# Kernel tuning notes

Measured on AMD Instinct MI355X. Metric: run time of the kernel, lower is better.

The kernel has to match this reference:

```python
import jax, jax.numpy as jnp
import numpy as np

FP, ENC, H, OUT, STEPS = 4860, 512, 512, 42, 128


def _lin(k, fan_in, fan_out, scale=0.02):
    kw, kb = jax.random.split(k)
    W = jax.random.normal(kw, (fan_out, fan_in), jnp.float32) * scale
    b = jax.random.normal(kb, (fan_out,), jnp.float32) * scale
    return W, b


def setup_inputs() -> dict:
    key = jax.random.key(0)
    ks = jax.random.split(key, 12)
    x = jax.random.normal(ks[0], (2048, FP), jnp.float32)
    y = jax.random.normal(ks[1], (2048, STEPS, OUT), jnp.float32)
    eps = jax.random.normal(ks[2], (2048, ENC), jnp.float32)
    We1, be1 = _lin(ks[3], FP, 2048)
    We2, be2 = _lin(ks[4], 2048, 1024)
    We3, be3 = _lin(ks[5], 1024, 512)
    We41, be41 = _lin(ks[6], 512, ENC)
    Wih, bih = _lin(ks[7], ENC, 3 * H)    # GRU input weights [3H, ENC]
    Whh, bhh = _lin(ks[8], H, 3 * H)      # GRU hidden weights [3H, H]
    Wf1, bf1 = _lin(ks[9], H, OUT)        # EncoderDecoder.fc1
    Wf2, bf2 = _lin(ks[10], OUT, H)       # EncoderDecoder.fc2
    return dict(x=x, y=y, eps=eps,
                We1=We1, be1=be1, We2=We2, be2=be2, We3=We3, be3=be3,
                We41=We41, be41=be41,
                Wih=Wih, bih=bih, Whh=Whh, bhh=bhh,
                Wf1=Wf1, bf1=bf1, Wf2=Wf2, bf2=bf2,
                teacher_forcing=0)


def _forward(x, eps, We1, be1, We2, be2, We3, be3, We41, be41,
             Wih, bih, Whh, bhh, Wf1, bf1, Wf2, bf2):
    # VAE encoder (note: source uses fc41 for BOTH mu and logvar)
    h1 = jax.nn.relu(x @ We1.T + be1)
    h2 = jax.nn.relu(h1 @ We2.T + be2)
    h3 = jax.nn.relu(h2 @ We3.T + be3)
    mu = h3 @ We41.T + be41
    logvar = mu
    encoded = eps * jnp.exp(0.5 * logvar) + mu  # reparameterize, [B, ENC]

    B = x.shape[0]
    h0 = jnp.zeros((B, H), x.dtype)

    def step(carry, _):
        h, xt = carry                      # h: [B,H], xt: [B,ENC]
        gi = xt @ Wih.T + bih              # [B,3H]
        gh = h @ Whh.T + bhh               # [B,3H]
        r = jax.nn.sigmoid(gi[:, :H] + gh[:, :H])
        z = jax.nn.sigmoid(gi[:, H:2 * H] + gh[:, H:2 * H])
        n = jnp.tanh(gi[:, 2 * H:] + r * gh[:, 2 * H:])
        h_new = (1.0 - z) * n + z * h
        out = jax.nn.relu(h_new @ Wf1.T + bf1)   # [B,42]
        x_new = jax.nn.relu(out @ Wf2.T + bf2)   # [B,H] (no teacher forcing)
        return (h_new, x_new), out

    (_, _), outs = jax.lax.scan(step, (h0, encoded), None, length=STEPS)
    return jnp.transpose(outs, (1, 0, 2))  # [B, 128, 42]


def reference(x, y, eps, We1, be1, We2, be2, We3, be3, We41, be41,
              Wih, bih, Whh, bhh, Wf1, bf1, Wf2, bf2, teacher_forcing):
    # teacher_forcing=0 (False path); y unused in that branch.
    return _forward(x, eps, We1, be1, We2, be2, We3, be3, We41, be41,
                    Wih, bih, Whh, bhh, Wf1, bf1, Wf2, bf2)
```

## Files before the change

### kernel.cpp

```cpp
#include <hip/hip_runtime.h>
#include <hip/hip_bf16.h>
#include <cstdint>
#include <cstddef>

#define DEVI __device__ __forceinline__

typedef __attribute__((ext_vector_type(8))) short bf16x8;
typedef __attribute__((ext_vector_type(4))) float f32x4;
typedef unsigned short u16;
typedef unsigned int u32;
typedef unsigned long long u64;

DEVI u16 f2bf(float f) {
    u32 i = __builtin_bit_cast(u32, f);
    u32 r = (i + 0x7FFFu + ((i >> 16) & 1u)) >> 16;
    return (u16)r;
}
DEVI float sigmoidf_(float x) { return 1.0f / (1.0f + __expf(-x)); }
DEVI float tanhf_(float x) { return 2.0f / (1.0f + __expf(-2.0f * x)) - 1.0f; }

typedef const __attribute__((address_space(1))) void* gptr_t;
typedef __attribute__((address_space(3))) void* lptr_t;

DEVI void gload16(const void* g, void* l) {
    __builtin_amdgcn_global_load_lds((gptr_t)g, (lptr_t)l, 16, 0, 0);
}

__global__ void fill_const(float* __restrict__ p, int n, float v) {
    int i = blockIdx.x * 256 + threadIdx.x;
    if (i < n) p[i] = v;
}

__global__ void cvt_pad(const float* __restrict__ src, u16* __restrict__ dst,
                        int wcols, int cols, int spitch, int dpitch) {
    int c = blockIdx.x * 256 + threadIdx.x;
    int r = blockIdx.y;
    if (c >= wcols) return;
    float v = (c < cols) ? src[(size_t)r * spitch + c] : 0.0f;
    dst[(size_t)r * dpitch + c] = f2bf(v);
}

__global__ void prep_wf1(const float* __restrict__ Wf1, u16* __restrict__ Wf1p) {
    int r = blockIdx.x;
    int c = threadIdx.x;
    Wf1p[r * 512 + c] = (r < 42) ? f2bf(Wf1[(size_t)r * 512 + c]) : (u16)0;
}
__global__ void prep_wf2(const float* __restrict__ Wf2, u16* __restrict__ Wf2p) {
    int c = blockIdx.x;
    int k = threadIdx.x;
    Wf2p[c * 64 + k] = (k < 42) ? f2bf(Wf2[(size_t)c * 42 + k]) : (u16)0;
}

template <int EPI>
__global__ __launch_bounds__(256) void gemm_bt(
    const u16* __restrict__ A, int lda, const u16* __restrict__ B, int ldb,
    const float* __restrict__ bias, u16* __restrict__ C, int ldc, int ktiles,
    const float* __restrict__ eps) {
    __shared__ u16 As[128 * 64];
    __shared__ u16 Bs[128 * 64];
    const int tid = threadIdx.x;
    const int lane = tid & 63;
    const int wave = tid >> 6;
    const int m0 = blockIdx.y * 128;
    const int n0 = blockIdx.x * 128;
    const int l15 = lane & 15, lg = lane >> 4;
    const int wm = (wave >> 1) * 64, wn = (wave & 1) * 64;

    f32x4 acc[4][4];
#pragma unroll
    for (int r = 0; r < 4; r++)
#pragma unroll
        for (int c = 0; c < 4; c++) acc[r][c] = (f32x4){0.f, 0.f, 0.f, 0.f};

    for (int t = 0; t < ktiles; ++t) {
        const int k0 = t * 64;
#pragma unroll
        for (int q = 0; q < 4; ++q) {
            int chunk = q * 4 + wave;
            int o = chunk * 1024 + lane * 16;
            int row = o >> 7;
            int cb = o & 127;
            gload16((const char*)(A + (size_t)(m0 + row) * lda + k0) + cb,
                    (char*)As + chunk * 1024);
            gload16((const char*)(B + (size_t)(n0 + row) * ldb + k0) + cb,
                    (char*)Bs + chunk * 1024);
        }
        __syncthreads();
#pragma unroll
        for (int kf = 0; kf < 2; ++kf) {
            bf16x8 a[4], b[4];
#pragma unroll
            for (int r = 0; r < 4; r++)
                a[r] = *(const bf16x8*)&As[(wm + 16 * r + l15) * 64 + kf * 32 + lg * 8];
#pragma unroll
            for (int c = 0; c < 4; c++)
                b[c] = *(const bf16x8*)&Bs[(wn + 16 * c + l15) * 64 + kf * 32 + lg * 8];
#pragma unroll
            for (int r = 0; r < 4; r++)
#pragma unroll
                for (int c = 0; c < 4; c++)
                    acc[r][c] = __builtin_amdgcn_mfma_f32_16x16x32_bf16(
                        a[r], b[c], acc[r][c], 0, 0, 0);
        }
        __syncthreads();
    }
#pragma unroll
    for (int r = 0; r < 4; r++) {
#pragma unroll
        for (int c = 0; c < 4; c++) {
            int col = n0 + wn + 16 * c + l15;
            float bv = bias[col];
#pragma unroll
            for (int i = 0; i < 4; i++) {
                int row = m0 + wm + 16 * r + lg * 4 + i;
                float v = acc[r][c][i] + bv;
                if (EPI == 0) {
                    v = v > 0.f ? v : 0.f;
                    C[(size_t)row * ldc + col] = f2bf(v);
                } else {
                    float e = eps[(size_t)row * 512 + col];
                    float enc = e * __expf(0.5f * v) + v;
                    C[(size_t)row * ldc + col] = f2bf(enc);
                }
            }
        }
    }
}

template <int MODE>
__global__ __launch_bounds__(256, 1) void gru_step(
    const u16* __restrict__ xt0, const u16* __restrict__ hbR,
    const float* __restrict__ hfR, u16* __restrict__ hbW,
    float* __restrict__ hfW, const u16* __restrict__ WB,
    const float* __restrict__ bih, const float* __restrict__ bhh,
    const u16* __restrict__ Wf1p, const float* __restrict__ bf1,
    const u16* __restrict__ Wf2p, const float* __restrict__ bf2,
    float* __restrict__ outp, int sidx) {
    __shared__ __align__(16) u16 xtL[64 * 512];
    __shared__ __align__(16) u16 Bst[192 * 64];
    __shared__ __align__(16) u16 oL[64 * 64];
    const int tid = threadIdx.x, lane = tid & 63, wave = tid >> 6;
    const int S = blockIdx.x * 64, m0 = blockIdx.y * 64;
    const int l15 = lane & 15, lg = lane >> 4;

    if (MODE == 0) {
        for (int q = 0; q < 16; ++q) {
            int row = wave * 16 + q;
            const char* src = (const char*)(xt0 + (size_t)(m0 + row) * 512) +
                              ((lane ^ (row & 7)) * 16);
            gload16(src, (char*)xtL + row * 1024);
        }
        __syncthreads();
    }

    if (MODE >= 1) {
        {
            int row = tid >> 2, part = tid & 3;
            int base = ((6 ^ (row & 7)) & ~1) * 16;
            *(u64*)((char*)oL + row * 128 + base + part * 8) = 0ull;
        }
        f32x4 oa[3];
#pragma unroll
        for (int c = 0; c < 3; c++) oa[c] = (f32x4){0.f, 0.f, 0.f, 0.f};
        const u16* hsrc = hbR + (size_t)(m0 + 16 * wave + l15) * 512 + lg * 8;
        const u16* w1src = Wf1p + (size_t)l15 * 512 + lg * 8;
#pragma unroll
        for (int kf = 0; kf < 16; ++kf) {
            bf16x8 a = *(const bf16x8*)(hsrc + kf * 32);
#pragma unroll
            for (int c = 0; c < 3; ++c) {
                bf16x8 b = *(const bf16x8*)(w1src + c * 16 * 512 + kf * 32);
                oa[c] = __builtin_amdgcn_mfma_f32_16x16x32_bf16(a, b, oa[c], 0, 0, 0);
            }
        }
#pragma unroll
        for (int c = 0; c < 3; ++c) {
            int col = 16 * c + l15;
            float bv = (col < 42) ? bf1[col] : 0.f;
#pragma unroll
            for (int i = 0; i < 4; ++i) {
                int lrow = 16 * wave + lg * 4 + i;
                float v = oa[c][i] + bv;
                v = v > 0.f ? v : 0.f;
                if (col >= 42) v = 0.f;
                int cb = col * 2;
                int byo = lrow * 128 + (((cb & ~15) ^ ((lrow & 7) << 4)) | (cb & 15));
                *(u16*)((char*)oL + byo) = f2bf(v);
                if (blockIdx.x == 0 && col < 42)
                    outp[(size_t)(m0 + lrow) * 5376 + (size_t)sidx * 42 + col] = v;
            }
        }
        __syncthreads();
    }

    if (MODE == 1) {
        f32x4 xa[32];
#pragma unroll
        for (int ct = 0; ct < 32; ct++) xa[ct] = (f32x4){0.f, 0.f, 0.f, 0.f};
        bf16x8 a2[2];
#pragma unroll
        for (int kf = 0; kf < 2; ++kf) {
            int row = 16 * wave + l15;
            int byo = row * 128 + ((kf * 64 + lg * 16) ^ ((row & 7) << 4));
            a2[kf] = *(const bf16x8*)((char*)oL + byo);
        }
#pragma unroll
        for (int ct = 0; ct < 32; ++ct) {
            const u16* wsrc = Wf2p + (size_t)(16 * ct + l15) * 64 + lg * 8;
#pragma unroll
            for (int kf = 0; kf < 2; ++kf) {
                bf16x8 b = *(const bf16x8*)(wsrc + kf * 32);
                xa[ct] = __builtin_amdgcn_mfma_f32_16x16x32_bf16(a2[kf], b, xa[ct], 0, 0, 0);
            }
        }
#pragma unroll
        for (int ct = 0; ct < 32; ++ct) {
            int col = 16 * ct + l15;
            float bv = bf2[col];
#pragma unroll
            for (int i = 0; i < 4; ++i) {
                int lrow = 16 * wave + lg * 4 + i;
                float v = xa[ct][i] + bv;
                v = v > 0.f ? v : 0.f;
                int cb = col * 2;
                int byo = lrow * 1024 + (((cb & ~15) ^ ((lrow & 7) << 4)) | (cb & 15));
                *(u16*)((char*)xtL + byo) = f2bf(v);
            }
        }
        __syncthreads();
    }

    if (MODE <= 1) {
        f32x4 ar[4], az[4], agi[4], agh[4];
#pragma unroll
        for (int c = 0; c < 4; c++) {
            ar[c] = (f32x4){0.f, 0.f, 0.f, 0.f};
            az[c] = (f32x4){0.f, 0.f, 0.f, 0.f};
            agi[c] = (f32x4){0.f, 0.f, 0.f, 0.f};
            agh[c] = (f32x4){0.f, 0.f, 0.f, 0.f};
        }
        const int arow = 16 * wave + l15;
        for (int t = 0; t < 16; ++t) {
#pragma unroll
            for (int q = 0; q < 6; ++q) {
                int ch = q * 4 + wave;
                int rowin = lane >> 3, sseg = lane & 7;
                int row = ch * 8 + rowin;
                int gate = row >> 6, unit = row & 63;
                const u16* src = WB + (size_t)(gate * 512 + S + unit) * 1024 +
                                 t * 64 + (sseg ^ rowin) * 8;
                gload16(src, (char*)Bst + ch * 1024);
            }
            __syncthreads();
            bf16x8 a[2];
#pragma unroll
            for (int kf = 0; kf < 2; ++kf) {
                if (t < 8) {
                    int byo = arow * 1024 +
                              ((t * 128 + kf * 64 + lg * 16) ^ ((arow & 7) << 4));
                    a[kf] = *(const bf16x8*)((char*)xtL + byo);
                } else {
                    a[kf] = *(const bf16x8*)(hbR + (size_t)(m0 + arow) * 512 +
                                             (t - 8) * 64 + kf * 32 + lg * 8);
                }
            }
#pragma unroll
            for (int kf = 0; kf < 2; ++kf) {
#pragma unroll
                for (int c = 0; c < 4; ++c) {
                    int brow = 16 * c + l15;
                    int kby = (kf * 64 + lg * 16) ^ ((brow & 7) << 4);
                    bf16x8 br = *(const bf16x8*)((char*)Bst + brow * 128 + kby);
                    bf16x8 bz = *(const bf16x8*)((char*)Bst + (64 + brow) * 128 + kby);
                    bf16x8 bn = *(const bf16x8*)((char*)Bst + (128 + brow) * 128 + kby);
                    ar[c] = __builtin_amdgcn_mfma_f32_16x16x32_bf16(a[kf], br, ar[c], 0, 0, 0);
                    az[c] = __builtin_amdgcn_mfma_f32_16x16x32_bf16(a[kf], bz, az[c], 0, 0, 0);
                    if (t < 8)
                        agi[c] = __builtin_amdgcn_mfma_f32_16x16x32_bf16(a[kf], bn, agi[c], 0, 0, 0);
                    else
                        agh[c] = __builtin_amdgcn_mfma_f32_16x16x32_bf16(a[kf], bn, agh[c], 0, 0, 0);
                }
            }
            __syncthreads();
        }
#pragma unroll
        for (int c = 0; c < 4; ++c) {
            int hu = S + 16 * c + l15;
            float br_ = bih[hu] + bhh[hu];
            float bz_ = bih[512 + hu] + bhh[512 + hu];
            float bgi = bih[1024 + hu];
            float bgh = bhh[1024 + hu];
#pragma unroll
            for (int i = 0; i < 4; ++i) {
                int grow = m0 + 16 * wave + lg * 4 + i;
                float rv = sigmoidf_(ar[c][i] + br_);
                float zv = sigmoidf_(az[c][i] + bz_);
                float nv = tanhf_(agi[c][i] + bgi + rv * (agh[c][i] + bgh));
                float hold = hfR[(size_t)grow * 512 + hu];
                float hn = (1.f - zv) * nv + zv * hold;
                hfW[(size_t)grow * 512 + hu] = hn;
                hbW[(size_t)grow * 512 + hu] = f2bf(hn);
            }
        }
    }
}

extern "C" void kernel_launch(void* const* d_in, const int* in_sizes, int n_in,
                              void* d_out, int out_size, void* d_ws,
                              size_t ws_size, hipStream_t stream) {
    (void)in_sizes; (void)n_in; (void)out_size;
    const float* x = (const float*)d_in[0];
    const float* eps = (const float*)d_in[2];
    const float* We1 = (const float*)d_in[3];
    const float* be1 = (const float*)d_in[4];
    const float* We2 = (const float*)d_in[5];
    const float* be2 = (const float*)d_in[6];
    const float* We3 = (const float*)d_in[7];
    const float* be3 = (const float*)d_in[8];
    const float* We41 = (const float*)d_in[9];
    const float* be41 = (const float*)d_in[10];
    const float* Wih = (const float*)d_in[11];
    const float* bih = (const float*)d_in[12];
    const float* Whh = (const float*)d_in[13];
    const float* bhh = (const float*)d_in[14];
    const float* Wf1 = (const float*)d_in[15];
    const float* bf1 = (const float*)d_in[16];
    const float* Wf2 = (const float*)d_in[17];
    const float* bf2 = (const float*)d_in[18];
    float* out = (float*)d_out;

    char* ws = (char*)d_ws;
    size_t off = 0;
    auto alloc = [&](size_t bytes) -> char* {
        char* p = ws + off;
        off += (bytes + 255) & ~(size_t)255;
        return p;
    };
    u16* xb = (u16*)alloc(2048ull * 4864 * 2);
    u16* We1b = (u16*)alloc(2048ull * 4864 * 2);
    u16* We2b = (u16*)alloc(1024ull * 2048 * 2);
    u16* We3b = (u16*)alloc(512ull * 1024 * 2);
    u16* We41b = (u16*)alloc(512ull * 512 * 2);
    u16* WB = (u16*)alloc(1536ull * 1024 * 2);
    u16* h1b = (u16*)alloc(2048ull * 2048 * 2);
    u16* h2b = (u16*)alloc(2048ull * 1024 * 2);
    u16* h3b = (u16*)alloc(2048ull * 512 * 2);
    u16* encb = (u16*)alloc(2048ull * 512 * 2);
    u16* hb0 = (u16*)alloc(2048ull * 512 * 2);
    u16* hb1 = (u16*)alloc(2048ull * 512 * 2);
    float* hf0 = (float*)alloc(2048ull * 512 * 4);
    float* hf1 = (float*)alloc(2048ull * 512 * 4);
    u16* Wf1p = (u16*)alloc(48ull * 512 * 2);
    u16* Wf2p = (u16*)alloc(512ull * 64 * 2);
    if (off > ws_size) {
        fill_const<<<(11010048 + 255) / 256, 256, 0, stream>>>(out, 11010048, 54321.0f);
        return;
    }
    u16* hb[2] = {hb0, hb1};
    float* hfl[2] = {hf0, hf1};

    auto cdiv = [](int a, int b) { return (a + b - 1) / b; };
    cvt_pad<<<dim3(cdiv(4864, 256), 2048), 256, 0, stream>>>(x, xb, 4864, 4860, 4860, 4864);
    cvt_pad<<<dim3(cdiv(4864, 256), 2048), 256, 0, stream>>>(We1, We1b, 4864, 4860, 4860, 4864);
    cvt_pad<<<dim3(cdiv(2048, 256), 1024), 256, 0, stream>>>(We2, We2b, 2048, 2048, 2048, 2048);
    cvt_pad<<<dim3(cdiv(1024, 256), 512), 256, 0, stream>>>(We3, We3b, 1024, 1024, 1024, 1024);
    cvt_pad<<<dim3(cdiv(512, 256), 512), 256, 0, stream>>>(We41, We41b, 512, 512, 512, 512);
    cvt_pad<<<dim3(cdiv(512, 256), 1536), 256, 0, stream>>>(Wih, WB, 512, 512, 512, 1024);
    cvt_pad<<<dim3(cdiv(512, 256), 1536), 256, 0, stream>>>(Whh, WB + 512, 512, 512, 512, 1024);
    prep_wf1<<<48, 512, 0, stream>>>(Wf1, Wf1p);
    prep_wf2<<<512, 64, 0, stream>>>(Wf2, Wf2p);
    hipMemsetAsync(hb0, 0, 2048ull * 512 * 2, stream);
    hipMemsetAsync(hf0, 0, 2048ull * 512 * 4, stream);

    gemm_bt<0><<<dim3(16, 16), 256, 0, stream>>>(xb, 4864, We1b, 4864, be1, h1b, 2048, 76, nullptr);
    gemm_bt<0><<<dim3(8, 16), 256, 0, stream>>>(h1b, 2048, We2b, 2048, be2, h2b, 1024, 32, nullptr);
    gemm_bt<0><<<dim3(4, 16), 256, 0, stream>>>(h2b, 1024, We3b, 1024, be3, h3b, 512, 16, nullptr);
    gemm_bt<1><<<dim3(4, 16), 256, 0, stream>>>(h3b, 512, We41b, 512, be41, encb, 512, 8, eps);

    gru_step<0><<<dim3(8, 32), 256, 0, stream>>>(encb, hb0, hf0, hb1, hf1, WB, bih,
                                                 bhh, Wf1p, bf1, Wf2p, bf2, out, 0);
    for (int i = 1; i < 128; ++i) {
        int p = i & 1;
        gru_step<1><<<dim3(8, 32), 256, 0, stream>>>(nullptr, hb[p], hfl[p],
                                                     hb[p ^ 1], hfl[p ^ 1], WB, bih,
                                                     bhh, Wf1p, bf1, Wf2p, bf2, out,
                                                     i - 1);
    }
    gru_step<2><<<dim3(1, 32), 256, 0, stream>>>(nullptr, hb0, hf0, nullptr, nullptr,
                                                 WB, bih, bhh, Wf1p, bf1, Wf2p, bf2,
                                                 out, 127);
}
```

Baseline: 5.103 ms.

## Widen GRU step blocks to 16 waves and double-buffer weight staging

The per-timestep GRU kernel goes from 4 to 16 waves per block. Each wave now owns a single 16x16 output tile rather than four, and the fc1/fc2 work is split across waves. Weight tiles are staged into two LDS buffers so the next k-slice loads while the current one is computed, and the hidden-state fragments are prefetched one iteration early. The aim is more latency hiding and shorter per-wave serial chains in the 128 launches that are latency-bound. In exchange there are more waves contending for one CU, more LDS, and an extra sync to zero the oL buffer.

Result: faster. 4.950 ms (-3.0%).

```diff
diff --git a/kernel.cpp b/kernel.cpp
--- a/kernel.cpp
+++ b/kernel.cpp
@@ -128,7 +128,7 @@
 }
 
 template <int MODE>
-__global__ __launch_bounds__(256, 1) void gru_step(
+__global__ __launch_bounds__(1024, 1) void gru_step(
     const u16* __restrict__ xt0, const u16* __restrict__ hbR,
     const float* __restrict__ hfR, u16* __restrict__ hbW,
     float* __restrict__ hfW, const u16* __restrict__ WB,
@@ -137,170 +137,166 @@
     const u16* __restrict__ Wf2p, const float* __restrict__ bf2,
     float* __restrict__ outp, int sidx) {
     __shared__ __align__(16) u16 xtL[64 * 512];
-    __shared__ __align__(16) u16 Bst[192 * 64];
+    __shared__ __align__(16) u16 Bst[2][192 * 64];
     __shared__ __align__(16) u16 oL[64 * 64];
     const int tid = threadIdx.x, lane = tid & 63, wave = tid >> 6;
+    const int wr = wave >> 2, wu = wave & 3;
+    const int l15 = lane & 15, lg = lane >> 4;
     const int S = blockIdx.x * 64, m0 = blockIdx.y * 64;
-    const int l15 = lane & 15, lg = lane >> 4;
 
     if (MODE == 0) {
-        for (int q = 0; q < 16; ++q) {
-            int row = wave * 16 + q;
-            const char* src = (const char*)(xt0 + (size_t)(m0 + row) * 512) +
-                              ((lane ^ (row & 7)) * 16);
-            gload16(src, (char*)xtL + row * 1024);
-        }
+#pragma unroll
+        for (int k2 = 0; k2 < 4; ++k2) {
+            int j = tid + k2 * 1024;
+            int row = j >> 6, slot = j & 63;
+            gload16((const char*)(xt0 + (size_t)(m0 + row) * 512) + (slot ^ (row & 7)) * 16,
+                    (char*)xtL + j * 16);
+        }
+    }
+
+    if (MODE >= 1) {
+        if (MODE == 1) {
+            ((u64*)oL)[tid] = 0ull;
+            __syncthreads();
+        }
+        if (wu < 3) {
+            f32x4 oa = (f32x4){0.f, 0.f, 0.f, 0.f};
+            const u16* ha = hbR + (size_t)(m0 + 16 * wr + l15) * 512 + lg * 8;
+            const u16* wb1 = Wf1p + (size_t)(16 * wu + l15) * 512 + lg * 8;
+#pragma unroll
+            for (int kf = 0; kf < 16; ++kf) {
+                bf16x8 a = *(const bf16x8*)(ha + kf * 32);
+                bf16x8 b = *(const bf16x8*)(wb1 + kf * 32);
+                oa = __builtin_amdgcn_mfma_f32_16x16x32_bf16(a, b, oa, 0, 0, 0);
+            }
+            int col = 16 * wu + l15;
+            float bv = (col < 42) ? bf1[col] : 0.f;
+#pragma unroll
+            for (int i = 0; i < 4; ++i) {
+                int row = 16 * wr + lg * 4 + i;
+                float v = oa[i] + bv;
+                v = v > 0.f ? v : 0.f;
+                if (MODE == 1) {
+                    int cb = col * 2;
+                    *(u16*)((char*)oL + row * 128 +
+                            (((cb & ~15) ^ ((row & 7) << 4)) | (cb & 15))) = f2bf(v);
+                }
+                if (blockIdx.x == 0 && col < 42)
+                    outp[(size_t)(m0 + row) * 5376 + (size_t)sidx * 42 + col] = v;
+            }
+        }
+    }
+
+    if (MODE == 1) {
         __syncthreads();
-    }
-
-    if (MODE >= 1) {
-        {
-            int row = tid >> 2, part = tid & 3;
-            int base = ((6 ^ (row & 7)) & ~1) * 16;
-            *(u64*)((char*)oL + row * 128 + base + part * 8) = 0ull;
-        }
-        f32x4 oa[3];
-#pragma unroll
-        for (int c = 0; c < 3; c++) oa[c] = (f32x4){0.f, 0.f, 0.f, 0.f};
-        const u16* hsrc = hbR + (size_t)(m0 + 16 * wave + l15) * 512 + lg * 8;
-        const u16* w1src = Wf1p + (size_t)l15 * 512 + lg * 8;
-#pragma unroll
-        for (int kf = 0; kf < 16; ++kf) {
-            bf16x8 a = *(const bf16x8*)(hsrc + kf * 32);
-#pragma unroll
-            for (int c = 0; c < 3; ++c) {
-                bf16x8 b = *(const bf16x8*)(w1src + c * 16 * 512 + kf * 32);
-                oa[c] = __builtin_amdgcn_mfma_f32_16x16x32_bf16(a, b, oa[c], 0, 0, 0);
-            }
-        }
-#pragma unroll
-        for (int c = 0; c < 3; ++c) {
-            int col = 16 * c + l15;
-            float bv = (col < 42) ? bf1[col] : 0.f;
+        bf16x8 a2[2];
+#pragma unroll
+        for (int kf = 0; kf < 2; ++kf) {
+            int row = 16 * wr + l15;
+            a2[kf] = *(const bf16x8*)((char*)oL + row * 128 +
+                                      ((kf * 64 + lg * 16) ^ ((row & 7) << 4)));
+        }
+#pragma unroll
+        for (int ci = 0; ci < 8; ++ci) {
+            int col = 128 * wu + 16 * ci + l15;
+            const u16* wb2 = Wf2p + (size_t)col * 64 + lg * 8;
+            f32x4 xa = (f32x4){0.f, 0.f, 0.f, 0.f};
+            xa = __builtin_amdgcn_mfma_f32_16x16x32_bf16(a2[0], *(const bf16x8*)wb2, xa, 0, 0, 0);
+            xa = __builtin_amdgcn_mfma_f32_16x16x32_bf16(a2[1], *(const bf16x8*)(wb2 + 32), xa, 0, 0, 0);
+            float bv = bf2[col];
+            int cb = col * 2;
 #pragma unroll
             for (int i = 0; i < 4; ++i) {
-                int lrow = 16 * wave + lg * 4 + i;
-                float v = oa[c][i] + bv;
+                int row = 16 * wr + lg * 4 + i;
+                float v = xa[i] + bv;
                 v = v > 0.f ? v : 0.f;
-                if (col >= 42) v = 0.f;
-                int cb = col * 2;
-                int byo = lrow * 128 + (((cb & ~15) ^ ((lrow & 7) << 4)) | (cb & 15));
-                *(u16*)((char*)oL + byo) = f2bf(v);
-                if (blockIdx.x == 0 && col < 42)
-                    outp[(size_t)(m0 + lrow) * 5376 + (size_t)sidx * 42 + col] = v;
-            }
-        }
+                *(u16*)((char*)xtL + row * 1024 +
+                        (((cb & ~15) ^ ((row & 7) << 4)) | (cb & 15))) = f2bf(v);
+            }
+        }
+    }
+
+    if (MODE <= 1) {
+        auto stageB = [&](int buf, int t) {
+            {
+                int j = tid;
+                int row = j >> 3, slot = j & 7;
+                int gate = row >> 6, unit = row & 63;
+                gload16(WB + (size_t)(gate * 512 + S + unit) * 1024 + t * 64 +
+                            (slot ^ (row & 7)) * 8,
+                        (char*)Bst + buf * 24576 + j * 16);
+            }
+            if (tid < 512) {
+                int j = tid + 1024;
+                int row = j >> 3, slot = j & 7;
+                int gate = row >> 6, unit = row & 63;
+                gload16(WB + (size_t)(gate * 512 + S + unit) * 1024 + t * 64 +
+                            (slot ^ (row & 7)) * 8,
+                        (char*)Bst + buf * 24576 + j * 16);
+            }
+        };
+        f32x4 ar = (f32x4){0.f, 0.f, 0.f, 0.f};
+        f32x4 az = ar, agi = ar, agh = ar;
+        const u16* hrow = hbR + (size_t)(m0 + 16 * wr + l15) * 512 + lg * 8;
+        bf16x8 hc0, hc1, hp0, hp1;
+
+        stageB(0, 0);
         __syncthreads();
-    }
-
-    if (MODE == 1) {
-        f32x4 xa[32];
-#pragma unroll
-        for (int ct = 0; ct < 32; ct++) xa[ct] = (f32x4){0.f, 0.f, 0.f, 0.f};
-        bf16x8 a2[2];
-#pragma unroll
-        for (int kf = 0; kf < 2; ++kf) {
-            int row = 16 * wave + l15;
-            int byo = row * 128 + ((kf * 64 + lg * 16) ^ ((row & 7) << 4));
-            a2[kf] = *(const bf16x8*)((char*)oL + byo);
-        }
-#pragma unroll
-        for (int ct = 0; ct < 32; ++ct) {
-            const u16* wsrc = Wf2p + (size_t)(16 * ct + l15) * 64 + lg * 8;
+
+        for (int t = 0; t < 16; ++t) {
+            if (t >= 7 && t < 15) {
+                const u16* hs = hrow + (t + 1 - 8) * 64;
+                hp0 = *(const bf16x8*)hs;
+                hp1 = *(const bf16x8*)(hs + 32);
+            }
+            if (t < 15) stageB((t + 1) & 1, t + 1);
+
+            bf16x8 a[2];
+            if (t < 8) {
+                int row = 16 * wr + l15;
+#pragma unroll
+                for (int kf = 0; kf < 2; ++kf)
+                    a[kf] = *(const bf16x8*)((char*)xtL + row * 1024 +
+                                             ((t * 128 + kf * 64 + lg * 16) ^ ((row & 7) << 4)));
+            } else {
+                a[0] = hc0;
+                a[1] = hc1;
+            }
+            const char* bb = (const char*)Bst + (t & 1) * 24576;
+            int rb0 = 16 * wu + l15;
+            int sw = (rb0 & 7) << 4;
 #pragma unroll
             for (int kf = 0; kf < 2; ++kf) {
-                bf16x8 b = *(const bf16x8*)(wsrc + kf * 32);
-                xa[ct] = __builtin_amdgcn_mfma_f32_16x16x32_bf16(a2[kf], b, xa[ct], 0, 0, 0);
-            }
-        }
-#pragma unroll
-        for (int ct = 0; ct < 32; ++ct) {
-            int col = 16 * ct + l15;
-            float bv = bf2[col];
-#pragma unroll
-            for (int i = 0; i < 4; ++i) {
-                int lrow = 16 * wave + lg * 4 + i;
-                float v = xa[ct][i] + bv;
-                v = v > 0.f ? v : 0.f;
-                int cb = col * 2;
-                int byo = lrow * 1024 + (((cb & ~15) ^ ((lrow & 7) << 4)) | (cb & 15));
-                *(u16*)((char*)xtL + byo) = f2bf(v);
-            }
-        }
-        __syncthreads();
-    }
-
-    if (MODE <= 1) {
-        f32x4 ar[4], az[4], agi[4], agh[4];
-#pragma unroll
-        for (int c = 0; c < 4; c++) {
-            ar[c] = (f32x4){0.f, 0.f, 0.f, 0.f};
-            az[c] = (f32x4){0.f, 0.f, 0.f, 0.f};
-            agi[c] = (f32x4){0.f, 0.f, 0.f, 0.f};
-            agh[c] = (f32x4){0.f, 0.f, 0.f, 0.f};
-        }
-        const int arow = 16 * wave + l15;
-        for (int t = 0; t < 16; ++t) {
-#pragma unroll
-            for (int q = 0; q < 6; ++q) {
-                int ch = q * 4 + wave;
-                int rowin = lane >> 3, sseg = lane & 7;
-                int row = ch * 8 + rowin;
-                int gate = row >> 6, unit = row & 63;
-                const u16* src = WB + (size_t)(gate * 512 + S + unit) * 1024 +
-                                 t * 64 + (sseg ^ rowin) * 8;
-                gload16(src, (char*)Bst + ch * 1024);
-            }
+                int kb = kf * 64 + lg * 16;
+                bf16x8 br = *(const bf16x8*)(bb + (size_t)rb0 * 128 + (kb ^ sw));
+                bf16x8 bz = *(const bf16x8*)(bb + (size_t)(64 + rb0) * 128 + (kb ^ sw));
+                bf16x8 bn = *(const bf16x8*)(bb + (size_t)(128 + rb0) * 128 + (kb ^ sw));
+                ar = __builtin_amdgcn_mfma_f32_16x16x32_bf16(a[kf], br, ar, 0, 0, 0);
+                az = __builtin_amdgcn_mfma_f32_16x16x32_bf16(a[kf], bz, az, 0, 0, 0);
+                if (t < 8)
+                    agi = __builtin_amdgcn_mfma_f32_16x16x32_bf16(a[kf], bn, agi, 0, 0, 0);
+                else
+                    agh = __builtin_amdgcn_mfma_f32_16x16x32_bf16(a[kf], bn, agh, 0, 0, 0);
+            }
+            hc0 = hp0;
+            hc1 = hp1;
             __syncthreads();
-            bf16x8 a[2];
-#pragma unroll
-            for (int kf = 0; kf < 2; ++kf) {
-                if (t < 8) {
-                    int byo = arow * 1024 +
-                              ((t * 128 + kf * 64 + lg * 16) ^ ((arow & 7) << 4));
-                    a[kf] = *(const bf16x8*)((char*)xtL + byo);
-                } else {
-                    a[kf] = *(const bf16x8*)(hbR + (size_t)(m0 + arow) * 512 +
-                                             (t - 8) * 64 + kf * 32 + lg * 8);
-                }
-            }
-#pragma unroll
-            for (int kf = 0; kf < 2; ++kf) {
-#pragma unroll
-                for (int c = 0; c < 4; ++c) {
-                    int brow = 16 * c + l15;
-                    int kby = (kf * 64 + lg * 16) ^ ((brow & 7) << 4);
-                    bf16x8 br = *(const bf16x8*)((char*)Bst + brow * 128 + kby);
-                    bf16x8 bz = *(const bf16x8*)((char*)Bst + (64 + brow) * 128 + kby);
-                    bf16x8 bn = *(const bf16x8*)((char*)Bst + (128 + brow) * 128 + kby);
-                    ar[c] = __builtin_amdgcn_mfma_f32_16x16x32_bf16(a[kf], br, ar[c], 0, 0, 0);
-                    az[c] = __builtin_amdgcn_mfma_f32_16x16x32_bf16(a[kf], bz, az[c], 0, 0, 0);
-                    if (t < 8)
-                        agi[c] = __builtin_amdgcn_mfma_f32_16x16x32_bf16(a[kf], bn, agi[c], 0, 0, 0);
-                    else
-                        agh[c] = __builtin_amdgcn_mfma_f32_16x16x32_bf16(a[kf], bn, agh[c], 0, 0, 0);
-                }
-            }
-            __syncthreads();
-        }
-#pragma unroll
-        for (int c = 0; c < 4; ++c) {
-            int hu = S + 16 * c + l15;
-            float br_ = bih[hu] + bhh[hu];
-            float bz_ = bih[512 + hu] + bhh[512 + hu];
-            float bgi = bih[1024 + hu];
-            float bgh = bhh[1024 + hu];
-#pragma unroll
-            for (int i = 0; i < 4; ++i) {
-                int grow = m0 + 16 * wave + lg * 4 + i;
-                float rv = sigmoidf_(ar[c][i] + br_);
-                float zv = sigmoidf_(az[c][i] + bz_);
-                float nv = tanhf_(agi[c][i] + bgi + rv * (agh[c][i] + bgh));
-                float hold = hfR[(size_t)grow * 512 + hu];
-                float hn = (1.f - zv) * nv + zv * hold;
-                hfW[(size_t)grow * 512 + hu] = hn;
-                hbW[(size_t)grow * 512 + hu] = f2bf(hn);
-            }
+        }
+        int hu = S + 16 * wu + l15;
+        float br_ = bih[hu] + bhh[hu];
+        float bz_ = bih[512 + hu] + bhh[512 + hu];
+        float bgi = bih[1024 + hu];
+        float bgh = bhh[1024 + hu];
+#pragma unroll
+        for (int i = 0; i < 4; ++i) {
+            int row = m0 + 16 * wr + lg * 4 + i;
+            float rv = sigmoidf_(ar[i] + br_);
+            float zv = sigmoidf_(az[i] + bz_);
+            float nv = tanhf_(agi[i] + bgi + rv * (agh[i] + bgh));
+            float hold = hfR[(size_t)row * 512 + hu];
+            float hn = (1.f - zv) * nv + zv * hold;
+            hfW[(size_t)row * 512 + hu] = hn;
+            hbW[(size_t)row * 512 + hu] = f2bf(hn);
         }
     }
 }
@@ -377,16 +373,16 @@
     gemm_bt<0><<<dim3(4, 16), 256, 0, stream>>>(h2b, 1024, We3b, 1024, be3, h3b, 512, 16, nullptr);
     gemm_bt<1><<<dim3(4, 16), 256, 0, stream>>>(h3b, 512, We41b, 512, be41, encb, 512, 8, eps);
 
-    gru_step<0><<<dim3(8, 32), 256, 0, stream>>>(encb, hb0, hf0, hb1, hf1, WB, bih,
-                                                 bhh, Wf1p, bf1, Wf2p, bf2, out, 0);
+    gru_step<0><<<dim3(8, 32), 1024, 0, stream>>>(encb, hb0, hf0, hb1, hf1, WB, bih,
+                                                  bhh, Wf1p, bf1, Wf2p, bf2, out, 0);
     for (int i = 1; i < 128; ++i) {
         int p = i & 1;
-        gru_step<1><<<dim3(8, 32), 256, 0, stream>>>(nullptr, hb[p], hfl[p],
-                                                     hb[p ^ 1], hfl[p ^ 1], WB, bih,
-                                                     bhh, Wf1p, bf1, Wf2p, bf2, out,
-                                                     i - 1);
-    }
-    gru_step<2><<<dim3(1, 32), 256, 0, stream>>>(nullptr, hb0, hf0, nullptr, nullptr,
-                                                 WB, bih, bhh, Wf1p, bf1, Wf2p, bf2,
-                                                 out, 127);
-}
+        gru_step<1><<<dim3(8, 32), 1024, 0, stream>>>(nullptr, hb[p], hfl[p],
+                                                      hb[p ^ 1], hfl[p ^ 1], WB, bih,
+                                                      bhh, Wf1p, bf1, Wf2p, bf2, out,
+                                                      i - 1);
+    }
+    gru_step<2><<<dim3(1, 32), 1024, 0, stream>>>(nullptr, hb0, hf0, nullptr, nullptr,
+                                                  WB, bih, bhh, Wf1p, bf1, Wf2p, bf2,
+                                                  out, 127);
+}
```
